# Optimization experiments

Hardware: AMD Instinct MI355X
Metric: run time of the kernel (lower is better)

Reference implementation:

```python
import jax, jax.numpy as jnp
import numpy as np

EMBED_DIM = 1024
NUM_HEADS = 16
HEAD_DIM = EMBED_DIM // NUM_HEADS
BATCH = 1  # module's torch.t(torch.squeeze(k)) requires batch==1
SEQ = 2048


def setup_inputs() -> dict:
    key = jax.random.key(0)
    k1, k2, k3, k4, k5 = jax.random.split(key, 5)
    s = 1.0 / np.sqrt(EMBED_DIM)
    return {
        "qkv": jax.random.normal(k1, (BATCH, SEQ, EMBED_DIM), jnp.float32),
        "w_in": jax.random.normal(k2, (EMBED_DIM, 3 * EMBED_DIM), jnp.float32) * s,
        "b_in": jax.random.normal(k3, (3 * EMBED_DIM,), jnp.float32) * 0.01,
        "w_out": jax.random.normal(k4, (EMBED_DIM, EMBED_DIM), jnp.float32) * s,
        "b_out": jax.random.normal(k5, (EMBED_DIM,), jnp.float32) * 0.01,
    }


def reference(qkv, w_in, b_in, w_out, b_out):
    B, S, E = qkv.shape
    H, D = NUM_HEADS, HEAD_DIM
    proj = qkv @ w_in + b_in                      # [B,S,3E]
    q, k, v = jnp.split(proj, 3, axis=2)          # each [B,S,E]
    q = q.reshape(B, S, H, D)
    k = k.reshape(B, S, H, D)
    v = v.reshape(B, S, H, D)
    scale = 1.0 / np.sqrt(D).astype(np.float32)
    scores = jnp.einsum("bshd,bthd->bhst", q, k) * scale  # [B,H,S,S]
    attn = jax.nn.softmax(scores, axis=-1)
    out = jnp.einsum("bhst,bthd->bshd", attn, v).reshape(B, S, E)
    return out @ w_out + b_out
```

## Files before the change

### kernel.cpp

```cpp
#include <hip/hip_runtime.h>
#include <math.h>

typedef short bf16x8 __attribute__((ext_vector_type(8)));
typedef _Float16 f16x8 __attribute__((ext_vector_type(8)));
typedef _Float16 f16x4 __attribute__((ext_vector_type(4)));
typedef float f32x4 __attribute__((ext_vector_type(4)));
typedef unsigned short u16x4 __attribute__((ext_vector_type(4)));

#define S_LEN 2048
#define E_DIM 1024
#define H_NUM 16
#define D_DIM 64
#define LDP   (3 * E_DIM)
#define QSCALE 0.18033688011112042f

#define MFMA16(a, b, c)  __builtin_amdgcn_mfma_f32_16x16x32_bf16((a), (b), (c), 0, 0, 0)
#define MFMA16H(a, b, c) __builtin_amdgcn_mfma_f32_16x16x32_f16((a), (b), (c), 0, 0, 0)

__device__ __forceinline__ unsigned short f2bf(float f) {
    union { float f; unsigned int u; } v; v.f = f;
    unsigned int r = v.u + 0x7FFFu + ((v.u >> 16) & 1u);
    return (unsigned short)(r >> 16);
}
__device__ __forceinline__ float exp2_fast(float x) {
    float r; asm("v_exp_f32 %0, %1" : "=v"(r) : "v"(x)); return r;
}
__device__ __forceinline__ unsigned int cvt_pk_bf16(float lo, float hi) {
    unsigned int r;
    asm("v_cvt_pk_bf16_f32 %0, %1, %2" : "=v"(r) : "v"(lo), "v"(hi));
    return r;
}
__device__ __forceinline__ void gl_lds16(const void* g, unsigned short* l) {
    __builtin_amdgcn_global_load_lds(
        (const __attribute__((address_space(1))) void*)g,
        (__attribute__((address_space(3))) void*)l, 16, 0, 0);
}

__global__ __launch_bounds__(256) void prep_kernel(
    const float* __restrict__ qkv, _Float16* __restrict__ Ah,
    const float* __restrict__ w_in, _Float16* __restrict__ Wt1,
    const float* __restrict__ w_out, _Float16* __restrict__ Wt2)
{
    __shared__ float tile[64][65];
    const int bid = blockIdx.x;
    const int t = threadIdx.x;

    if (bid < 2048) {
        const int i = bid * 256 + t;
        const float4 v = ((const float4*)qkv)[i];
        f16x4 hh;
        hh[0] = (_Float16)v.x; hh[1] = (_Float16)v.y;
        hh[2] = (_Float16)v.z; hh[3] = (_Float16)v.w;
        ((f16x4*)Ah)[i] = hh;
        return;
    }
    const float* B;
    _Float16* Bt;
    int bx, by, N;
    if (bid < 2816) { B = w_in;  Bt = Wt1; N = 3 * E_DIM; bx = (bid - 2048) % 48; by = (bid - 2048) / 48; }
    else            { B = w_out; Bt = Wt2; N = E_DIM;     bx = (bid - 2816) % 16; by = (bid - 2816) / 16; }
    const int K = E_DIM;
    const int k0 = by * 64, n0 = bx * 64;
    const int r4 = t >> 6, c = t & 63;
#pragma unroll
    for (int rep = 0; rep < 16; ++rep)
        tile[rep * 4 + r4][c] = B[(size_t)(k0 + rep * 4 + r4) * N + n0 + c];
    __syncthreads();
#pragma unroll
    for (int rep = 0; rep < 16; ++rep) {
        const int n = rep * 4 + r4;
        Bt[(size_t)(n0 + n) * K + k0 + c] = (_Float16)tile[c][n];
    }
}

template <int BM, int BN, int OUT_MODE, int TWO_PASS>
__global__ __launch_bounds__(256) void gemm_f16_kernel(
    const _Float16* __restrict__ Ah, const _Float16* __restrict__ Al,
    const _Float16* __restrict__ Bt, const float* __restrict__ bias,
    void* __restrict__ Cout, int M, int N, int K, int nbx)
{
    constexpr int AROWS = TWO_PASS ? 2 * BM : BM;
    constexpr int ROWS = AROWS + BN;
    constexpr int NISS = ROWS / 16;
    constexpr int MI = BM / 32, NI = BN / 32;
    __shared__ unsigned short lds[2 * ROWS * 32];

    const int nwg = gridDim.x;
    const int bid = blockIdx.x;
    const int qch = nwg >> 3;
    const int swz = (bid & 7) * qch + (bid >> 3);
    const int n0 = (swz % nbx) * BN;
    const int m0 = (swz / nbx) * BM;

    const int t = threadIdx.x;
    const int wid = t >> 6, lane = t & 63;
    const int wr = wid >> 1, wc = wid & 1;
    const int lc = lane & 15, g = lane >> 4;
    const int lrow = lane >> 2;
    const int lcol = (lane & 3) * 8;

    f32x4 acc[MI][NI];
    const f32x4 zf = {0.f, 0.f, 0.f, 0.f};
#pragma unroll
    for (int mi = 0; mi < MI; ++mi)
#pragma unroll
        for (int ni = 0; ni < NI; ++ni) acc[mi][ni] = zf;

    auto stage = [&](int k0, int b) {
        unsigned short* base = &lds[b * ROWS * 32];
#pragma unroll
        for (int e = wid; e < NISS; e += 4) {
            const int rb = e * 16;
            const int rr = rb + lrow;
            const _Float16* gp;
            if (rb < BM)                            gp = &Ah[(size_t)(m0 + rr) * K + k0 + lcol];
            else if (TWO_PASS && rb < 2 * BM)       gp = &Al[(size_t)(m0 + rr - BM) * K + k0 + lcol];
            else                                    gp = &Bt[(size_t)(n0 + rr - AROWS) * K + k0 + lcol];
            gl_lds16(gp, base + rb * 32);
        }
    };

    stage(0, 0);
    const int NK = K / 32;
    for (int ks = 0; ks < NK; ++ks) {
        __syncthreads();
        if (ks + 1 < NK) stage((ks + 1) * 32, (ks + 1) & 1);
        const unsigned short* cb = &lds[(ks & 1) * ROWS * 32];

        f16x8 bfr[NI];
#pragma unroll
        for (int ni = 0; ni < NI; ++ni)
            bfr[ni] = *(const f16x8*)&cb[(AROWS + wc * (BN / 2) + ni * 16 + lc) * 32 + g * 8];
#pragma unroll
        for (int mi = 0; mi < MI; ++mi) {
            const int ar = wr * (BM / 2) + mi * 16 + lc;
            const f16x8 ah = *(const f16x8*)&cb[ar * 32 + g * 8];
#pragma unroll
            for (int ni = 0; ni < NI; ++ni)
                acc[mi][ni] = MFMA16H(ah, bfr[ni], acc[mi][ni]);
            if (TWO_PASS) {
                const f16x8 al = *(const f16x8*)&cb[(BM + ar) * 32 + g * 8];
#pragma unroll
                for (int ni = 0; ni < NI; ++ni)
                    acc[mi][ni] = MFMA16H(al, bfr[ni], acc[mi][ni]);
            }
        }
    }

#pragma unroll
    for (int ni = 0; ni < NI; ++ni) {
        const int col = n0 + wc * (BN / 2) + ni * 16 + lc;
        const float bv = bias[col];
        float sc = 1.f;
        if (OUT_MODE == 1) sc = (col < E_DIM) ? QSCALE : 1.f;
#pragma unroll
        for (int mi = 0; mi < MI; ++mi) {
            const int rbase = m0 + wr * (BM / 2) + mi * 16 + g * 4;
#pragma unroll
            for (int i = 0; i < 4; ++i) {
                const float v = acc[mi][ni][i] + bv;
                if (OUT_MODE == 1)
                    ((unsigned short*)Cout)[(size_t)(rbase + i) * N + col] = f2bf(v * sc);
                else
                    ((float*)Cout)[(size_t)(rbase + i) * N + col] = v;
            }
        }
    }
}

__global__ __launch_bounds__(512, 4) void attn_mfma_kernel(
    const unsigned short* __restrict__ proj, _Float16* __restrict__ Oh)
{
    __shared__ unsigned short lds[20480];
    float* ldsf = (float*)lds;
    const int Q_OFF = 16384;

    const int t = threadIdx.x;
    const int w = t >> 6, lane = t & 63;
    const int lc = lane & 15, g = lane >> 4;
    const int qg = w & 3;
    const int half = w >> 2;
    const int ts = t & 255;

    const int bid = blockIdx.x;
    const int swb = (bid & 7) * 64 + (bid >> 3);
    const int qt = swb & 31;
    const int h  = swb >> 5;
    const int q0 = qt * 64;

    const size_t qoff = (size_t)h * D_DIM;
    const size_t koff = E_DIM + (size_t)h * D_DIM;
    const size_t voff = 2 * E_DIM + (size_t)h * D_DIM;

    const int KO = half * 4096;
    const int VO = 8192 + half * 4096;
    const int kvbase = half * (S_LEN / 2);

    const int r  = ts >> 2;
    const int s  = (ts & 3) * 16;
    const int sw = (r & 7) << 3;
    const int kv = (ts & 15) * 4;
    const int d0 = (ts >> 4) * 4;

    uint4 ka, kb;
    u16x4 vr[4];
    auto load_kv = [&](int tile) {
        const int t0 = kvbase + tile * 64;
        const unsigned short* gk = &proj[(size_t)(t0 + r) * LDP + koff + s];
        ka = ((const uint4*)gk)[0];
        kb = ((const uint4*)gk)[1];
#pragma unroll
        for (int r2 = 0; r2 < 4; ++r2)
            vr[r2] = *(const u16x4*)&proj[(size_t)(t0 + kv + r2) * LDP + voff + d0];
    };
    auto store_kv = [&]() {
        *(uint4*)&lds[KO + r * 64 + (s ^ sw)]       = ka;
        *(uint4*)&lds[KO + r * 64 + ((s + 8) ^ sw)] = kb;
#pragma unroll
        for (int j = 0; j < 4; ++j) {
            u16x4 w4; w4[0] = vr[0][j]; w4[1] = vr[1][j]; w4[2] = vr[2][j]; w4[3] = vr[3][j];
            const int d = d0 + j;
            *(u16x4*)&lds[VO + d * 64 + (kv ^ ((d & 7) << 3))] = w4;
        }
    };

    if (half == 0) {
        const unsigned short* gq = &proj[(size_t)(q0 + r) * LDP + qoff + s];
        const uint4 v0 = ((const uint4*)gq)[0];
        const uint4 v1 = ((const uint4*)gq)[1];
        *(uint4*)&lds[Q_OFF + r * 64 + (s ^ sw)]       = v0;
        *(uint4*)&lds[Q_OFF + r * 64 + ((s + 8) ^ sw)] = v1;
    }
    load_kv(0);
    store_kv();
    __syncthreads();

    bf16x8 qB0, qB1;
    {
        const int rq = qg * 16 + lc;
        const int swq = (rq & 7) << 3;
        qB0 = *(const bf16x8*)&lds[Q_OFF + rq * 64 + ((g * 8) ^ swq)];
        qB1 = *(const bf16x8*)&lds[Q_OFF + rq * 64 + ((32 + g * 8) ^ swq)];
    }
    __syncthreads();

    f32x4 oacc[4];
    const f32x4 zf = {0.f, 0.f, 0.f, 0.f};
#pragma unroll
    for (int i = 0; i < 4; ++i) oacc[i] = zf;
    float mrun = -1e30f;
    float lsum = 0.f;

    const int pb = Q_OFF + w * 512 + lc * 32;
    const int psw = ((lc >> 1) & 3) << 3;

    const int NTH = (S_LEN / 2) / 64;
    for (int tt = 0; tt < NTH; ++tt) {
        if (tt + 1 < NTH) load_kv(tt + 1);

        f32x4 sacc[4];
#pragma unroll
        for (int c = 0; c < 4; ++c) sacc[c] = zf;
        __builtin_amdgcn_s_setprio(1);
#pragma unroll
        for (int c = 0; c < 4; ++c) {
            const int kr = c * 16 + lc;
            const int swk = (kr & 7) << 3;
            const bf16x8 kf = *(const bf16x8*)&lds[KO + kr * 64 + ((g * 8) ^ swk)];
            sacc[c] = MFMA16(kf, qB0, sacc[c]);
        }
#pragma unroll
        for (int c = 0; c < 4; ++c) {
            const int kr = c * 16 + lc;
            const int swk = (kr & 7) << 3;
            const bf16x8 kf = *(const bf16x8*)&lds[KO + kr * 64 + ((32 + g * 8) ^ swk)];
            sacc[c] = MFMA16(kf, qB1, sacc[c]);
        }
        __builtin_amdgcn_s_setprio(0);

        float lmax = fmaxf(fmaxf(sacc[0][0], sacc[0][1]), fmaxf(sacc[0][2], sacc[0][3]));
        lmax = fmaxf(lmax, fmaxf(fmaxf(sacc[1][0], sacc[1][1]), fmaxf(sacc[1][2], sacc[1][3])));
        lmax = fmaxf(lmax, fmaxf(fmaxf(sacc[2][0], sacc[2][1]), fmaxf(sacc[2][2], sacc[2][3])));
        lmax = fmaxf(lmax, fmaxf(fmaxf(sacc[3][0], sacc[3][1]), fmaxf(sacc[3][2], sacc[3][3])));
        if (__any(lmax > mrun + 8.0f)) {
            float mx = lmax;
            mx = fmaxf(mx, __shfl_xor(mx, 16));
            mx = fmaxf(mx, __shfl_xor(mx, 32));
            const float mnew = fmaxf(mrun, mx);
            const float fs = exp2_fast(mrun - mnew);
            lsum *= fs;
            mrun = mnew;
#pragma unroll
            for (int i = 0; i < 4; ++i) {
                const float fsi = __shfl(fs, 4 * g + i, 16);
                oacc[0][i] *= fsi; oacc[1][i] *= fsi;
                oacc[2][i] *= fsi; oacc[3][i] *= fsi;
            }
        }

#pragma unroll
        for (int c = 0; c < 4; ++c)
#pragma unroll
            for (int i = 0; i < 4; ++i)
                sacc[c][i] = exp2_fast(sacc[c][i] - mrun);
        lsum += ((sacc[0][0] + sacc[0][1]) + (sacc[0][2] + sacc[0][3]))
              + ((sacc[1][0] + sacc[1][1]) + (sacc[1][2] + sacc[1][3]))
              + ((sacc[2][0] + sacc[2][1]) + (sacc[2][2] + sacc[2][3]))
              + ((sacc[3][0] + sacc[3][1]) + (sacc[3][2] + sacc[3][3]));

#pragma unroll
        for (int hf = 0; hf < 2; ++hf) {
#pragma unroll
            for (int c2 = 0; c2 < 2; ++c2) {
                const int c = hf * 2 + c2;
                uint2 w2;
                w2.x = cvt_pk_bf16(sacc[c][0], sacc[c][1]);
                w2.y = cvt_pk_bf16(sacc[c][2], sacc[c][3]);
                *(uint2*)&lds[pb + ((c2 * 16 + 4 * g) ^ psw)] = w2;
            }
            const bf16x8 pA = *(const bf16x8*)&lds[pb + ((g * 8) ^ psw)];
            __builtin_amdgcn_s_setprio(1);
#pragma unroll
            for (int dt = 0; dt < 4; ++dt) {
                const int vrow = dt * 16 + lc;
                const int swv = (vrow & 7) << 3;
                const bf16x8 vB = *(const bf16x8*)&lds[VO + vrow * 64 + ((hf * 32 + g * 8) ^ swv)];
                oacc[dt] = MFMA16(pA, vB, oacc[dt]);
            }
            __builtin_amdgcn_s_setprio(0);
        }

        __syncthreads();
        if (tt + 1 < NTH) {
            store_kv();
            __syncthreads();
        }
    }

    float ps = lsum;
    ps += __shfl_xor(ps, 16);
    ps += __shfl_xor(ps, 32);

    if (half == 1) {
#pragma unroll
        for (int dt = 0; dt < 4; ++dt)
#pragma unroll
            for (int i = 0; i < 4; ++i)
                ldsf[qg * 1024 + (dt * 4 + i) * 64 + lane] = oacc[dt][i];
        ldsf[4096 + qg * 128 + lane] = mrun;
        ldsf[4096 + qg * 128 + 64 + lane] = ps;
    }
    __syncthreads();
    if (half == 0) {
        const float m2 = ldsf[4096 + qg * 128 + lane];
        const float l2 = ldsf[4096 + qg * 128 + 64 + lane];
        const float mf = fmaxf(mrun, m2);
        const float f1 = exp2_fast(mrun - mf);
        const float f2 = exp2_fast(m2 - mf);
        const float inv = 1.f / (ps * f1 + l2 * f2);
#pragma unroll
        for (int i = 0; i < 4; ++i) {
            const float f1i = __shfl(f1, 4 * g + i, 16);
            const float f2i = __shfl(f2, 4 * g + i, 16);
            const float invi = __shfl(inv, 4 * g + i, 16);
            const int row = q0 + qg * 16 + 4 * g + i;
#pragma unroll
            for (int dt = 0; dt < 4; ++dt) {
                const float o2 = ldsf[qg * 1024 + (dt * 4 + i) * 64 + lane];
                const float x = (oacc[dt][i] * f1i + o2 * f2i) * invi;
                Oh[(size_t)row * E_DIM + h * D_DIM + dt * 16 + lc] = (_Float16)x;
            }
        }
    }
}

extern "C" void kernel_launch(void* const* d_in, const int* in_sizes, int n_in,
                              void* d_out, int out_size, void* d_ws, size_t ws_size,
                              hipStream_t stream)
{
    (void)in_sizes; (void)n_in; (void)out_size; (void)ws_size;

    const float* qkv   = (const float*)d_in[0];
    const float* w_in  = (const float*)d_in[1];
    const float* b_in  = (const float*)d_in[2];
    const float* w_out = (const float*)d_in[3];
    const float* b_out = (const float*)d_in[4];
    float* out = (float*)d_out;

    unsigned char* ws = (unsigned char*)d_ws;
    _Float16* Wt1 = (_Float16*)(ws);
    _Float16* Wt2 = (_Float16*)(ws + 6291456);
    _Float16* Ah1 = (_Float16*)(ws + 8388608);
    unsigned short* proj = (unsigned short*)(ws + 16777216);
    _Float16* Oh = Ah1;

    prep_kernel<<<3072, 256, 0, stream>>>(qkv, Ah1, w_in, Wt1, w_out, Wt2);

    gemm_f16_kernel<128, 96, 1, 0><<<512, 256, 0, stream>>>(
        Ah1, Ah1, Wt1, b_in, (void*)proj, S_LEN, 3 * E_DIM, E_DIM, 32);

    attn_mfma_kernel<<<512, 512, 0, stream>>>(proj, Oh);

    gemm_f16_kernel<64, 64, 0, 0><<<512, 256, 0, stream>>>(
        Oh, Oh, Wt2, b_out, (void*)out, S_LEN, E_DIM, E_DIM, 16);
}
```

Baseline: 86.70 us.

## Split attention KV range across two blocks and merge partial outputs

Splits each head/query-tile's key-value range into two halves processed by separate blocks, doubling the attention grid to 1024 blocks. Each block writes a normalized partial output plus a log-sum-exp value. A new merge kernel combines the two partials. This is meant to raise parallelism and occupancy on the GPU's compute units, at the cost of extra global traffic for the partial outputs, an extra kernel launch, and shorter per-block loops with less latency amortisation.

```diff
diff --git a/kernel.cpp b/kernel.cpp
--- a/kernel.cpp
+++ b/kernel.cpp
@@ -169,7 +169,9 @@
 }
 
 __global__ __launch_bounds__(512, 4) void attn_mfma_kernel(
-    const unsigned short* __restrict__ proj, _Float16* __restrict__ Oh)
+    const unsigned short* __restrict__ proj,
+    _Float16* __restrict__ O0, _Float16* __restrict__ O1,
+    float* __restrict__ mstar)
 {
     __shared__ unsigned short lds[20480];
     float* ldsf = (float*)lds;
@@ -183,10 +185,11 @@
     const int ts = t & 255;
 
     const int bid = blockIdx.x;
-    const int swb = (bid & 7) * 64 + (bid >> 3);
-    const int qt = swb & 31;
-    const int h  = swb >> 5;
-    const int q0 = qt * 64;
+    const int swb = (bid & 7) * 128 + (bid >> 3);
+    const int h   = swb >> 6;
+    const int ks  = (swb >> 5) & 1;
+    const int qt  = swb & 31;
+    const int q0  = qt * 64;
 
     const size_t qoff = (size_t)h * D_DIM;
     const size_t koff = E_DIM + (size_t)h * D_DIM;
@@ -194,7 +197,7 @@
 
     const int KO = half * 4096;
     const int VO = 8192 + half * 4096;
-    const int kvbase = half * (S_LEN / 2);
+    const int kvbase = ks * 1024 + half * 512;
 
     const int r  = ts >> 2;
     const int s  = (ts & 3) * 16;
@@ -254,7 +257,7 @@
     const int pb = Q_OFF + w * 512 + lc * 32;
     const int psw = ((lc >> 1) & 3) << 3;
 
-    const int NTH = (S_LEN / 2) / 64;
+    const int NTH = 512 / 64;
     for (int tt = 0; tt < NTH; ++tt) {
         if (tt + 1 < NTH) load_kv(tt + 1);
 
@@ -357,7 +360,12 @@
         const float mf = fmaxf(mrun, m2);
         const float f1 = exp2_fast(mrun - mf);
         const float f2 = exp2_fast(m2 - mf);
-        const float inv = 1.f / (ps * f1 + l2 * f2);
+        const float L = ps * f1 + l2 * f2;
+        const float inv = 1.f / L;
+        if (g == 0)
+            mstar[(size_t)ks * S_LEN * H_NUM + (size_t)(q0 + qg * 16 + lc) * H_NUM + h]
+                = mf + __log2f(L);
+        _Float16* Op = ks ? O1 : O0;
 #pragma unroll
         for (int i = 0; i < 4; ++i) {
             const float f1i = __shfl(f1, 4 * g + i, 16);
@@ -368,10 +376,33 @@
             for (int dt = 0; dt < 4; ++dt) {
                 const float o2 = ldsf[qg * 1024 + (dt * 4 + i) * 64 + lane];
                 const float x = (oacc[dt][i] * f1i + o2 * f2i) * invi;
-                Oh[(size_t)row * E_DIM + h * D_DIM + dt * 16 + lc] = (_Float16)x;
-            }
-        }
-    }
+                Op[(size_t)row * E_DIM + h * D_DIM + dt * 16 + lc] = (_Float16)x;
+            }
+        }
+    }
+}
+
+__global__ __launch_bounds__(256) void merge_kernel(
+    const _Float16* __restrict__ O0, const _Float16* __restrict__ O1,
+    const float* __restrict__ mstar, _Float16* __restrict__ Oh)
+{
+    const int idx = blockIdx.x * 256 + threadIdx.x;
+    const int row = idx >> 7;
+    const int c8  = idx & 127;
+    const int h   = c8 >> 3;
+    const float m0 = mstar[(size_t)row * H_NUM + h];
+    const float m1 = mstar[(size_t)S_LEN * H_NUM + (size_t)row * H_NUM + h];
+    const float mf = fmaxf(m0, m1);
+    const float w0 = exp2_fast(m0 - mf);
+    const float w1 = exp2_fast(m1 - mf);
+    const float inv = 1.f / (w0 + w1);
+    const f16x8 a = ((const f16x8*)O0)[idx];
+    const f16x8 b = ((const f16x8*)O1)[idx];
+    f16x8 o;
+#pragma unroll
+    for (int j = 0; j < 8; ++j)
+        o[j] = (_Float16)(((float)a[j] * w0 + (float)b[j] * w1) * inv);
+    ((f16x8*)Oh)[idx] = o;
 }
 
 extern "C" void kernel_launch(void* const* d_in, const int* in_sizes, int n_in,
@@ -391,15 +422,20 @@
     _Float16* Wt1 = (_Float16*)(ws);
     _Float16* Wt2 = (_Float16*)(ws + 6291456);
     _Float16* Ah1 = (_Float16*)(ws + 8388608);
-    unsigned short* proj = (unsigned short*)(ws + 16777216);
-    _Float16* Oh = Ah1;
+    unsigned short* proj = (unsigned short*)(ws + 12582912);
+    _Float16* O0    = (_Float16*)(ws);
+    float*    mstar = (float*)(ws + 4194304);
+    _Float16* O1    = (_Float16*)(ws + 25165824);
+    _Float16* Oh    = Ah1;
 
     prep_kernel<<<3072, 256, 0, stream>>>(qkv, Ah1, w_in, Wt1, w_out, Wt2);
 
     gemm_f16_kernel<128, 96, 1, 0><<<512, 256, 0, stream>>>(
         Ah1, Ah1, Wt1, b_in, (void*)proj, S_LEN, 3 * E_DIM, E_DIM, 32);
 
-    attn_mfma_kernel<<<512, 512, 0, stream>>>(proj, Oh);
+    attn_mfma_kernel<<<1024, 512, 0, stream>>>(proj, O0, O1, mstar);
+
+    merge_kernel<<<1024, 256, 0, stream>>>(O0, O1, mstar, Oh);
 
     gemm_f16_kernel<64, 64, 0, 0><<<512, 256, 0, stream>>>(
         Oh, Oh, Wt2, b_out, (void*)out, S_LEN, E_DIM, E_DIM, 16);
```

New measurement: 91.39 us. 1.05x slower.
